# Optimization experiments

Measured on AMD Instinct MI355X. Metric: run time of the kernel, lower is better.

The kernel has to match this reference:

```python
import jax, jax.numpy as jnp
import numpy as np

D = 1024
H = 16
T_BLOCK = 2048


def setup_inputs() -> dict:
    key = jax.random.key(0)
    ks = jax.random.split(key, 12)
    B, T = 2, 2048
    s = lambda k, shape: jax.random.normal(k, shape, jnp.float32) * 0.02
    return {
        "x": jax.random.normal(ks[0], (B, T, D), jnp.float32),
        # layernorms
        "ln1_g": jnp.ones((D,), jnp.float32), "ln1_b": jnp.zeros((D,), jnp.float32),
        "ln2_g": jnp.ones((D,), jnp.float32), "ln2_b": jnp.zeros((D,), jnp.float32),
        # attention qkv projection ([in,out] layout) and output proj
        "w_qkv": s(ks[1], (D, 3 * D)), "b_qkv": jnp.zeros((3 * D,), jnp.float32),
        "w_o": s(ks[2], (D, D)), "b_o": jnp.zeros((D,), jnp.float32),
        # MLP
        "w_fc1": s(ks[3], (D, 4 * D)), "b_fc1": jnp.zeros((4 * D,), jnp.float32),
        "w_fc2": s(ks[4], (4 * D, D)), "b_fc2": jnp.zeros((D,), jnp.float32),
    }


def _layernorm(x, g, b, eps=1e-5):
    mu = jnp.mean(x, axis=-1, keepdims=True)
    var = jnp.var(x, axis=-1, keepdims=True)
    return (x - mu) * jax.lax.rsqrt(var + eps) * g + b


def _attention(x, w_qkv, b_qkv, w_o, b_o):
    B, T, C = x.shape
    hd = C // H
    qkv = x @ w_qkv + b_qkv                      # [B,T,3C]
    q, k, v = jnp.split(qkv, 3, axis=-1)
    split = lambda t: t.reshape(B, T, H, hd).transpose(0, 2, 1, 3)  # [B,H,T,hd]
    q, k, v = split(q), split(k), split(v)
    att = jnp.einsum("bhqd,bhkd->bhqk", q, k) / jnp.sqrt(jnp.float32(hd))
    causal = jnp.tril(jnp.ones((T, T), bool))
    att = jnp.where(causal[None, None], att, -jnp.inf)
    att = jax.nn.softmax(att, axis=-1)
    y = jnp.einsum("bhqk,bhkd->bhqd", att, v)    # [B,H,T,hd]
    y = y.transpose(0, 2, 1, 3).reshape(B, T, C)
    return y @ w_o + b_o


def reference(x, ln1_g, ln1_b, ln2_g, ln2_b, w_qkv, b_qkv, w_o, b_o,
              w_fc1, b_fc1, w_fc2, b_fc2):
    # dropout is identity in eval mode
    x = x + _attention(_layernorm(x, ln1_g, ln1_b), w_qkv, b_qkv, w_o, b_o)
    h = jax.nn.gelu(_layernorm(x, ln2_g, ln2_b) @ w_fc1 + b_fc1)
    return x + (h @ w_fc2 + b_fc2)
```

## Files before the change

kernel.cpp:

```cpp
#include <hip/hip_runtime.h>
#include <hip/hip_bf16.h>


using bf16 = __bf16;
using bf16x8 = __attribute__((ext_vector_type(8))) __bf16;
using floatx4 = __attribute__((ext_vector_type(4))) float;

#define D_ 1024
#define T_ 2048
#define B_ 2
#define H_ 16

static __device__ __forceinline__ bf16 f2bf(float f) { return (bf16)f; }

static __device__ __forceinline__ void async16(const void* g, void* l) {
  __builtin_amdgcn_global_load_lds(
      (const __attribute__((address_space(1))) void*)g,
      (__attribute__((address_space(3))) void*)l, 16, 0, 0);
}

static __device__ __forceinline__ float gelu_f(float v) {
  const float u2 = 1.5957691216057308f * (v + 0.044715f * v * v * v);
  return v / (1.0f + __expf(-u2));
}

__global__ void transpose_cast_all(const float* __restrict__ w_qkv,
                                   const float* __restrict__ w_o,
                                   const float* __restrict__ w_fc1,
                                   const float* __restrict__ w_fc2,
                                   bf16* __restrict__ wqkvT, bf16* __restrict__ woT,
                                   bf16* __restrict__ wfc1T, bf16* __restrict__ wfc2T) {
  int t = blockIdx.x;
  const float* in;
  bf16* out;
  int K, N, nx;
  if (t < 3072)      { in = w_qkv; out = wqkvT; K = 1024; N = 3072; nx = 96;  }
  else if (t < 4096) { in = w_o;   out = woT;   K = 1024; N = 1024; nx = 32;  t -= 3072; }
  else if (t < 8192) { in = w_fc1; out = wfc1T; K = 1024; N = 4096; nx = 128; t -= 4096; }
  else               { in = w_fc2; out = wfc2T; K = 4096; N = 1024; nx = 32;  t -= 8192; }
  const int n0 = (t % nx) * 32, k0 = (t / nx) * 32;
  __shared__ float tile[32][33];
  const int tx = threadIdx.x, ty = threadIdx.y;
  for (int i = 0; i < 32; i += 8)
    tile[ty + i][tx] = in[(size_t)(k0 + ty + i) * N + n0 + tx];
  __syncthreads();
  for (int i = 0; i < 32; i += 8)
    out[(size_t)(n0 + ty + i) * K + k0 + tx] = f2bf(tile[tx][ty + i]);
}

__global__ __launch_bounds__(256)
void ln_kernel(const float* __restrict__ x, const float* __restrict__ g,
               const float* __restrict__ bsh, bf16* __restrict__ out) {
  const int row = blockIdx.x, tid = threadIdx.x;
  const float4 v = ((const float4*)(x + (size_t)row * D_))[tid];
  float s = v.x + v.y + v.z + v.w;
  float s2 = v.x * v.x + v.y * v.y + v.z * v.z + v.w * v.w;
  for (int off = 32; off; off >>= 1) {
    s += __shfl_xor(s, off);
    s2 += __shfl_xor(s2, off);
  }
  __shared__ float red[8];
  const int wave = tid >> 6, lane = tid & 63;
  if (lane == 0) { red[wave] = s; red[wave + 4] = s2; }
  __syncthreads();
  s = red[0] + red[1] + red[2] + red[3];
  s2 = red[4] + red[5] + red[6] + red[7];
  const float mu = s * (1.0f / D_);
  const float rstd = rsqrtf(s2 * (1.0f / D_) - mu * mu + 1e-5f);
  const float4 gv = ((const float4*)g)[tid];
  const float4 bv = ((const float4*)bsh)[tid];
  bf16 o[4] __attribute__((aligned(8)));
  o[0] = f2bf((v.x - mu) * rstd * gv.x + bv.x);
  o[1] = f2bf((v.y - mu) * rstd * gv.y + bv.y);
  o[2] = f2bf((v.z - mu) * rstd * gv.z + bv.z);
  o[3] = f2bf((v.w - mu) * rstd * gv.w + bv.w);
  *(ushort4*)(out + (size_t)row * D_ + tid * 4) = *(const ushort4*)o;
}

template <int EPI>
__global__ __launch_bounds__(256)
void gemm_bt_sb(const bf16* __restrict__ A, const bf16* __restrict__ Bt,
                const float* __restrict__ bias, const float* __restrict__ res,
                void* __restrict__ Cout, int M, int N, int K) {
  __shared__ __align__(16) bf16 As[128][64];
  __shared__ __align__(16) bf16 Bs[128][64];
  const int tid = threadIdx.x;
  const int wave = tid >> 6, lane = tid & 63;
  const int quad = lane >> 4, l16 = lane & 15;
  const int wr = wave >> 1, wc = wave & 1;
  const int bm = blockIdx.x * 128, bn = blockIdx.y * 128;
  const int lrow8 = lane >> 3;
  const int lcol = (((lane & 7) ^ lrow8) * 8);

  floatx4 acc[4][4] = {};

  for (int k0 = 0; k0 < K; k0 += 64) {
    __syncthreads();
    for (int c = 0; c < 4; c++) {
      const int r = wave * 32 + c * 8;
      async16(&A[(size_t)(bm + r + lrow8) * K + k0 + lcol], &As[r][0]);
      async16(&Bt[(size_t)(bn + r + lrow8) * K + k0 + lcol], &Bs[r][0]);
    }
    __syncthreads();
    for (int ks = 0; ks < 2; ks++) {
      const int fc = ((quad + ks * 4) ^ (l16 & 7)) * 8;
      bf16x8 af[4], bfr[4];
      for (int mt = 0; mt < 4; mt++)
        af[mt] = *(const bf16x8*)&As[wr * 64 + mt * 16 + l16][fc];
      for (int nt = 0; nt < 4; nt++)
        bfr[nt] = *(const bf16x8*)&Bs[wc * 64 + nt * 16 + l16][fc];
      for (int mt = 0; mt < 4; mt++)
        for (int nt = 0; nt < 4; nt++)
          acc[mt][nt] = __builtin_amdgcn_mfma_f32_16x16x32_bf16(
              af[mt], bfr[nt], acc[mt][nt], 0, 0, 0);
    }
  }

  for (int mt = 0; mt < 4; mt++) {
    for (int nt = 0; nt < 4; nt++) {
      const int col = bn + wc * 64 + nt * 16 + l16;
      const float bcol = bias[col];
      for (int i = 0; i < 4; i++) {
        const int row = bm + wr * 64 + mt * 16 + quad * 4 + i;
        float v = acc[mt][nt][i] + bcol;
        if (EPI == 0) {
          ((bf16*)Cout)[(size_t)row * N + col] = f2bf(v);
        } else if (EPI == 1) {
          ((bf16*)Cout)[(size_t)row * N + col] = f2bf(gelu_f(v));
        } else {
          ((float*)Cout)[(size_t)row * N + col] = v + res[(size_t)row * N + col];
        }
      }
    }
  }
}

template <int EPI>
__global__ __launch_bounds__(256)
void gemm_bt(const bf16* __restrict__ A, const bf16* __restrict__ Bt,
             const float* __restrict__ bias, const float* __restrict__ res,
             void* __restrict__ Cout, int M, int N, int K) {
  __shared__ __align__(16) bf16 As[2][128][64];
  __shared__ __align__(16) bf16 Bs[2][128][64];
  const int tid = threadIdx.x;
  const int wave = tid >> 6, lane = tid & 63;
  const int quad = lane >> 4, l16 = lane & 15;
  const int wr = wave >> 1, wc = wave & 1;
  const int bm = blockIdx.x * 128, bn = blockIdx.y * 128;
  const int lrow8 = lane >> 3;
  const int lcol = (((lane & 7) ^ lrow8) * 8);

  const bf16* aBase = &A[(size_t)(bm + wave * 32 + lrow8) * K + lcol];
  const bf16* bBase = &Bt[(size_t)(bn + wave * 32 + lrow8) * K + lcol];

  auto stage = [&](int buf, int kk) {
    const int k0 = kk * 64;
    for (int c = 0; c < 4; c++) {
      async16(aBase + (size_t)c * 8 * K + k0, &As[buf][wave * 32 + c * 8][0]);
      async16(bBase + (size_t)c * 8 * K + k0, &Bs[buf][wave * 32 + c * 8][0]);
    }
  };

  floatx4 acc[4][4] = {};
  const int nsteps = K >> 6;

  stage(0, 0);
  if (nsteps > 1) stage(1, 1);
  int cur = 0;
  for (int t = 0; t < nsteps; ++t) {
    if (t < nsteps - 1)
      asm volatile("s_waitcnt vmcnt(8)" ::: "memory");
    else
      asm volatile("s_waitcnt vmcnt(0)" ::: "memory");
    __builtin_amdgcn_s_barrier();
    __builtin_amdgcn_sched_barrier(0);
    for (int ks = 0; ks < 2; ks++) {
      const int fc = ((quad + ks * 4) ^ (l16 & 7)) * 8;
      bf16x8 af[4], bfr[4];
      for (int mt = 0; mt < 4; mt++)
        af[mt] = *(const bf16x8*)&As[cur][wr * 64 + mt * 16 + l16][fc];
      for (int nn = 0; nn < 4; nn++)
        bfr[nn] = *(const bf16x8*)&Bs[cur][wc * 64 + nn * 16 + l16][fc];
      for (int mt = 0; mt < 4; mt++)
        for (int nn = 0; nn < 4; nn++)
          acc[mt][nn] = __builtin_amdgcn_mfma_f32_16x16x32_bf16(
              af[mt], bfr[nn], acc[mt][nn], 0, 0, 0);
    }
    __builtin_amdgcn_sched_barrier(0);
    __builtin_amdgcn_s_barrier();
    if (t + 2 < nsteps) stage(cur, t + 2);
    cur ^= 1;
  }

  for (int mt = 0; mt < 4; mt++) {
    for (int nn = 0; nn < 4; nn++) {
      const int col = bn + wc * 64 + nn * 16 + l16;
      const float bcol = bias[col];
      for (int i = 0; i < 4; i++) {
        const int row = bm + wr * 64 + mt * 16 + quad * 4 + i;
        float v = acc[mt][nn][i] + bcol;
        if (EPI == 0) {
          ((bf16*)Cout)[(size_t)row * N + col] = f2bf(v);
        } else if (EPI == 1) {
          ((bf16*)Cout)[(size_t)row * N + col] = f2bf(gelu_f(v));
        } else {
          ((float*)Cout)[(size_t)row * N + col] = v + res[(size_t)row * N + col];
        }
      }
    }
  }
}

template <int EPI>
__global__ __launch_bounds__(256)
void gemm64_dbuf(const bf16* __restrict__ A, const bf16* __restrict__ Bt,
                 const float* __restrict__ bias, const float* __restrict__ res,
                 void* __restrict__ Cout, int M, int N, int K) {
  __shared__ __align__(16) bf16 As[2][64][64];
  __shared__ __align__(16) bf16 Bs[2][128][64];
  const int tid = threadIdx.x;
  const int wave = tid >> 6, lane = tid & 63;
  const int quad = lane >> 4, l16 = lane & 15;
  const int wr = wave >> 1, wc = wave & 1;
  const int bm = blockIdx.x * 64, bn = blockIdx.y * 128;
  const int lrow8 = lane >> 3;
  const int lcol = (((lane & 7) ^ lrow8) * 8);

  const bf16* aBase = &A[(size_t)(bm + wave * 16 + lrow8) * K + lcol];
  const bf16* bBase = &Bt[(size_t)(bn + wave * 32 + lrow8) * K + lcol];

  auto stage = [&](int buf, int kk) {
    const int k0 = kk * 64;
    for (int c = 0; c < 2; c++)
      async16(aBase + (size_t)c * 8 * K + k0, &As[buf][wave * 16 + c * 8][0]);
    for (int c = 0; c < 4; c++)
      async16(bBase + (size_t)c * 8 * K + k0, &Bs[buf][wave * 32 + c * 8][0]);
  };

  floatx4 acc[2][4] = {};
  const int nsteps = K >> 6;

  stage(0, 0);
  if (nsteps > 1) stage(1, 1);
  int cur = 0;
  for (int t = 0; t < nsteps; ++t) {
    if (t < nsteps - 1)
      asm volatile("s_waitcnt vmcnt(6)" ::: "memory");
    else
      asm volatile("s_waitcnt vmcnt(0)" ::: "memory");
    __builtin_amdgcn_s_barrier();
    __builtin_amdgcn_sched_barrier(0);
    for (int ks = 0; ks < 2; ks++) {
      const int fc = ((quad + ks * 4) ^ (l16 & 7)) * 8;
      bf16x8 af[2], bfr[4];
      for (int mt = 0; mt < 2; mt++)
        af[mt] = *(const bf16x8*)&As[cur][wr * 32 + mt * 16 + l16][fc];
      for (int nt = 0; nt < 4; nt++)
        bfr[nt] = *(const bf16x8*)&Bs[cur][wc * 64 + nt * 16 + l16][fc];
      for (int mt = 0; mt < 2; mt++)
        for (int nt = 0; nt < 4; nt++)
          acc[mt][nt] = __builtin_amdgcn_mfma_f32_16x16x32_bf16(
              af[mt], bfr[nt], acc[mt][nt], 0, 0, 0);
    }
    __builtin_amdgcn_sched_barrier(0);
    __builtin_amdgcn_s_barrier();
    if (t + 2 < nsteps) stage(cur, t + 2);
    cur ^= 1;
  }

  for (int mt = 0; mt < 2; mt++) {
    for (int nt = 0; nt < 4; nt++) {
      const int col = bn + wc * 64 + nt * 16 + l16;
      const float bcol = bias[col];
      for (int i = 0; i < 4; i++) {
        const int row = bm + wr * 32 + mt * 16 + quad * 4 + i;
        float v = acc[mt][nt][i] + bcol;
        if (EPI == 0) {
          ((bf16*)Cout)[(size_t)row * N + col] = f2bf(v);
        } else if (EPI == 1) {
          ((bf16*)Cout)[(size_t)row * N + col] = f2bf(gelu_f(v));
        } else {
          ((float*)Cout)[(size_t)row * N + col] = v + res[(size_t)row * N + col];
        }
      }
    }
  }
}

__global__ __launch_bounds__(512)
void attn_kernel(const bf16* __restrict__ qkv, bf16* __restrict__ y) {
  const int bh = blockIdx.y, b = bh >> 4, h = bh & 15;
  const int tile = (blockIdx.y & 16) ? (int)blockIdx.x : (15 - (int)blockIdx.x);
  const int q0 = tile * 128;
  const int tid = threadIdx.x, wave = tid >> 6, lane = tid & 63;
  const int quad = lane >> 4, l16 = lane & 15;
  const int l7 = l16 & 7;
  const int w16 = wave * 16;

  __shared__ __align__(16) bf16 Ks[64][64];
  __shared__ __align__(16) bf16 Vts[64][64];
  __shared__ __align__(16) bf16 Ps[128][64];

  const size_t bbase = (size_t)b * T_ * 3072 + (size_t)h * 64;
  const bf16* Qg = qkv + bbase;
  const bf16* Kg = qkv + bbase + 1024;
  const bf16* Vg = qkv + bbase + 2048;

  bf16x8 ones;
  for (int j = 0; j < 8; j++) ones[j] = f2bf(1.0f);

  const int kr = tid >> 3, kch = tid & 7;
  const int kcol = ((kch ^ (kr & 7)) * 8);
  const int vk = tid & 63, vd = tid >> 6;

  bf16x8 qf[2];
  for (int ks = 0; ks < 2; ks++) {
    bf16x8 t = *(const bf16x8*)
        &Qg[(size_t)(q0 + w16 + l16) * 3072 + ks * 32 + quad * 8];
    for (int j = 0; j < 8; j++) t[j] = f2bf((float)t[j] * 0.125f);
    qf[ks] = t;
  }

  int4 kreg = *(const int4*)&Kg[(size_t)kr * 3072 + kch * 8];
  bf16x8 vreg = *(const bf16x8*)&Vg[(size_t)vk * 3072 + vd * 8];

  floatx4 accY[4] = {};
  floatx4 accL = {};

  const int kend = q0 + 64;
  for (int kc = 0; kc <= kend; kc += 64) {
    __syncthreads();
    *(int4*)&Ks[kr][kcol] = kreg;
    for (int j = 0; j < 8; j++) {
      const int d = vd * 8 + j;
      Vts[d][((vk >> 3) ^ j) * 8 + (vk & 7)] = vreg[j];
    }
    __syncthreads();

    if (kc < kend) {
      kreg = *(const int4*)&Kg[(size_t)(kc + 64 + kr) * 3072 + kch * 8];
      vreg = *(const bf16x8*)&Vg[(size_t)(kc + 64 + vk) * 3072 + vd * 8];
    }

    floatx4 s[4];
    for (int nt = 0; nt < 4; nt++) {
      const bf16* krow = &Ks[nt * 16 + l16][0];
      bf16x8 kf0 = *(const bf16x8*)&krow[(quad ^ l7) * 8];
      bf16x8 kf1 = *(const bf16x8*)&krow[((4 + quad) ^ l7) * 8];
      floatx4 t = {};
      t = __builtin_amdgcn_mfma_f32_16x16x32_bf16(qf[0], kf0, t, 0, 0, 0);
      t = __builtin_amdgcn_mfma_f32_16x16x32_bf16(qf[1], kf1, t, 0, 0, 0);
      s[nt] = t;
    }
    if (kc + 64 > q0 + w16) {
      for (int nt = 0; nt < 4; nt++)
        for (int i = 0; i < 4; i++) {
          const int c = kc + nt * 16 + l16;
          const int r = q0 + w16 + quad * 4 + i;
          if (c > r) s[nt][i] = -1e30f;
        }
    }

    for (int i = 0; i < 4; i++) {
      const int pr = quad * 4 + i;
      bf16* prow = &Ps[w16 + pr][0];
      for (int nt = 0; nt < 4; nt++)
        prow[(((nt * 2 + (l16 >> 3)) ^ (pr & 7)) * 8) + l7] =
            f2bf(__expf(s[nt][i] - 8.0f));
    }
    __builtin_amdgcn_wave_barrier();

    for (int ks = 0; ks < 2; ks++) {
      bf16x8 pa = *(const bf16x8*)&Ps[w16 + l16][((ks * 4 + quad) ^ l7) * 8];
      for (int dt = 0; dt < 4; dt++) {
        bf16x8 vb = *(const bf16x8*)&Vts[dt * 16 + l16][((ks * 4 + quad) ^ l7) * 8];
        accY[dt] =
            __builtin_amdgcn_mfma_f32_16x16x32_bf16(pa, vb, accY[dt], 0, 0, 0);
      }
      accL = __builtin_amdgcn_mfma_f32_16x16x32_bf16(pa, ones, accL, 0, 0, 0);
    }
  }

  for (int i = 0; i < 4; i++) {
    const float linv = 1.0f / accL[i];
    const int r = q0 + w16 + quad * 4 + i;
    for (int dt = 0; dt < 4; dt++)
      y[(size_t)(b * T_ + r) * D_ + h * 64 + dt * 16 + l16] =
          f2bf(accY[dt][i] * linv);
  }
}

extern "C" void kernel_launch(void* const* d_in, const int* in_sizes, int n_in,
                              void* d_out, int out_size, void* d_ws, size_t ws_size,
                              hipStream_t stream) {
  const float* x     = (const float*)d_in[0];
  const float* ln1_g = (const float*)d_in[1];
  const float* ln1_b = (const float*)d_in[2];
  const float* ln2_g = (const float*)d_in[3];
  const float* ln2_b = (const float*)d_in[4];
  const float* w_qkv = (const float*)d_in[5];
  const float* b_qkv = (const float*)d_in[6];
  const float* w_o   = (const float*)d_in[7];
  const float* b_o   = (const float*)d_in[8];
  const float* w_fc1 = (const float*)d_in[9];
  const float* b_fc1 = (const float*)d_in[10];
  const float* w_fc2 = (const float*)d_in[11];
  const float* b_fc2 = (const float*)d_in[12];

  char* p = (char*)d_ws;
  bf16* wqkvT = (bf16*)p; p += (size_t)3072 * 1024 * 2;
  bf16* woT   = (bf16*)p; p += (size_t)1024 * 1024 * 2;
  bf16* wfc1T = (bf16*)p; p += (size_t)4096 * 1024 * 2;
  bf16* wfc2T = (bf16*)p; p += (size_t)1024 * 4096 * 2;
  bf16* ln1   = (bf16*)p; p += (size_t)4096 * 1024 * 2;
  bf16* qkv   = (bf16*)p; p += (size_t)4096 * 3072 * 2;
  bf16* yb    = (bf16*)p; p += (size_t)4096 * 1024 * 2;
  float* x2   = (float*)p; p += (size_t)4096 * 1024 * 4;
  bf16* ln2   = (bf16*)p; p += (size_t)4096 * 1024 * 2;
  bf16* hb    = (bf16*)p; p += (size_t)4096 * 4096 * 2;

  transpose_cast_all<<<dim3(12288), dim3(32, 8), 0, stream>>>(
      w_qkv, w_o, w_fc1, w_fc2, wqkvT, woT, wfc1T, wfc2T);

  ln_kernel<<<4096, 256, 0, stream>>>(x, ln1_g, ln1_b, ln1);
  gemm_bt_sb<0><<<dim3(32, 24), 256, 0, stream>>>(ln1, wqkvT, b_qkv, nullptr, qkv,
                                                  4096, 3072, 1024);
  attn_kernel<<<dim3(16, 32), 512, 0, stream>>>(qkv, yb);
  gemm64_dbuf<2><<<dim3(64, 8), 256, 0, stream>>>(yb, woT, b_o, x, x2,
                                                  4096, 1024, 1024);
  ln_kernel<<<4096, 256, 0, stream>>>(x2, ln2_g, ln2_b, ln2);
  gemm_bt<1><<<dim3(32, 32), 256, 0, stream>>>(ln2, wfc1T, b_fc1, nullptr, hb,
                                               4096, 4096, 1024);
  gemm64_dbuf<2><<<dim3(64, 8), 256, 0, stream>>>(hb, wfc2T, b_fc2, x2, (float*)d_out,
                                                  4096, 1024, 4096);
}
```

Before: 315.4 us.

## Replace double-buffered K64 GEMM with single-buffered K128 tile loop

Output-projection and fc2 GEMMs now stage 128-wide K tiles into a single LDS buffer with a wider XOR swizzle, instead of double-buffering 64-wide tiles with explicit vmcnt waits. This halves the number of loop iterations and barriers per tile of work. In exchange, global loads no longer overlap with MFMA compute, since each iteration waits for its loads before computing.

Result: no change. 309.9 us (-1.7%).

```diff
diff --git a/kernel.cpp b/kernel.cpp
--- a/kernel.cpp
+++ b/kernel.cpp
@@ -213,59 +213,46 @@
 
 template <int EPI>
 __global__ __launch_bounds__(256)
-void gemm64_dbuf(const bf16* __restrict__ A, const bf16* __restrict__ Bt,
+void gemm64_k128(const bf16* __restrict__ A, const bf16* __restrict__ Bt,
                  const float* __restrict__ bias, const float* __restrict__ res,
                  void* __restrict__ Cout, int M, int N, int K) {
-  __shared__ __align__(16) bf16 As[2][64][64];
-  __shared__ __align__(16) bf16 Bs[2][128][64];
+  __shared__ __align__(16) bf16 As[64][128];
+  __shared__ __align__(16) bf16 Bs[128][128];
   const int tid = threadIdx.x;
   const int wave = tid >> 6, lane = tid & 63;
   const int quad = lane >> 4, l16 = lane & 15;
   const int wr = wave >> 1, wc = wave & 1;
   const int bm = blockIdx.x * 64, bn = blockIdx.y * 128;
-  const int lrow8 = lane >> 3;
-  const int lcol = (((lane & 7) ^ lrow8) * 8);
-
-  const bf16* aBase = &A[(size_t)(bm + wave * 16 + lrow8) * K + lcol];
-  const bf16* bBase = &Bt[(size_t)(bn + wave * 32 + lrow8) * K + lcol];
-
-  auto stage = [&](int buf, int kk) {
-    const int k0 = kk * 64;
-    for (int c = 0; c < 2; c++)
-      async16(aBase + (size_t)c * 8 * K + k0, &As[buf][wave * 16 + c * 8][0]);
-    for (int c = 0; c < 4; c++)
-      async16(bBase + (size_t)c * 8 * K + k0, &Bs[buf][wave * 32 + c * 8][0]);
-  };
+  const int sr = lane >> 4;
+  const int pchunk = lane & 15;
 
   floatx4 acc[2][4] = {};
-  const int nsteps = K >> 6;
-
-  stage(0, 0);
-  if (nsteps > 1) stage(1, 1);
-  int cur = 0;
-  for (int t = 0; t < nsteps; ++t) {
-    if (t < nsteps - 1)
-      asm volatile("s_waitcnt vmcnt(6)" ::: "memory");
-    else
-      asm volatile("s_waitcnt vmcnt(0)" ::: "memory");
-    __builtin_amdgcn_s_barrier();
-    __builtin_amdgcn_sched_barrier(0);
-    for (int ks = 0; ks < 2; ks++) {
-      const int fc = ((quad + ks * 4) ^ (l16 & 7)) * 8;
+
+  for (int k0 = 0; k0 < K; k0 += 128) {
+    __syncthreads();
+    for (int c = 0; c < 4; c++) {
+      const int base = wave * 16 + c * 4;
+      const int scol = (pchunk ^ ((c * 4 + sr) & 15)) * 8;
+      async16(&A[(size_t)(bm + base + sr) * K + k0 + scol], &As[base][0]);
+    }
+    for (int c = 0; c < 8; c++) {
+      const int base = wave * 32 + c * 4;
+      const int scol = (pchunk ^ ((c * 4 + sr) & 15)) * 8;
+      async16(&Bt[(size_t)(bn + base + sr) * K + k0 + scol], &Bs[base][0]);
+    }
+    __syncthreads();
+    for (int ks = 0; ks < 4; ks++) {
+      const int fc = ((quad + ks * 4) ^ l16) * 8;
       bf16x8 af[2], bfr[4];
       for (int mt = 0; mt < 2; mt++)
-        af[mt] = *(const bf16x8*)&As[cur][wr * 32 + mt * 16 + l16][fc];
+        af[mt] = *(const bf16x8*)&As[wr * 32 + mt * 16 + l16][fc];
       for (int nt = 0; nt < 4; nt++)
-        bfr[nt] = *(const bf16x8*)&Bs[cur][wc * 64 + nt * 16 + l16][fc];
+        bfr[nt] = *(const bf16x8*)&Bs[wc * 64 + nt * 16 + l16][fc];
       for (int mt = 0; mt < 2; mt++)
         for (int nt = 0; nt < 4; nt++)
           acc[mt][nt] = __builtin_amdgcn_mfma_f32_16x16x32_bf16(
               af[mt], bfr[nt], acc[mt][nt], 0, 0, 0);
     }
-    __builtin_amdgcn_sched_barrier(0);
-    __builtin_amdgcn_s_barrier();
-    if (t + 2 < nsteps) stage(cur, t + 2);
-    cur ^= 1;
   }
 
   for (int mt = 0; mt < 2; mt++) {
@@ -426,11 +413,11 @@
   gemm_bt_sb<0><<<dim3(32, 24), 256, 0, stream>>>(ln1, wqkvT, b_qkv, nullptr, qkv,
                                                   4096, 3072, 1024);
   attn_kernel<<<dim3(16, 32), 512, 0, stream>>>(qkv, yb);
-  gemm64_dbuf<2><<<dim3(64, 8), 256, 0, stream>>>(yb, woT, b_o, x, x2,
+  gemm64_k128<2><<<dim3(64, 8), 256, 0, stream>>>(yb, woT, b_o, x, x2,
                                                   4096, 1024, 1024);
   ln_kernel<<<4096, 256, 0, stream>>>(x2, ln2_g, ln2_b, ln2);
   gemm_bt<1><<<dim3(32, 32), 256, 0, stream>>>(ln2, wfc1T, b_fc1, nullptr, hb,
                                                4096, 4096, 1024);
-  gemm64_dbuf<2><<<dim3(64, 8), 256, 0, stream>>>(hb, wfc2T, b_fc2, x2, (float*)d_out,
+  gemm64_k128<2><<<dim3(64, 8), 256, 0, stream>>>(hb, wfc2T, b_fc2, x2, (float*)d_out,
                                                   4096, 1024, 4096);
 }
```
